# Kernel optimization log

Hardware: AMD Instinct MI355X
Metric: run time of the kernel (lower is better)

Reference implementation:

```python
import jax, jax.numpy as jnp
import numpy as np

NUM_HEADS = 4


def setup_inputs() -> dict:
    key = jax.random.key(0)
    ks = jax.random.split(key, 5)
    B, S, E = 32, 1024, 512
    T, Q = 128, 256
    src_encodings = jax.random.normal(ks[0], (B, S, E), dtype=jnp.float32)
    src_token_mask = jax.random.randint(ks[1], (B, S), 0, 2).astype(bool)
    query_vec = jax.random.normal(ks[2], (T, B, Q), dtype=jnp.float32)
    # torch Linear weights are (out_features, in_features)
    W_src = jax.random.normal(ks[3], (NUM_HEADS * Q, E), dtype=jnp.float32) * (1.0 / np.sqrt(E))
    W_opt = jax.random.normal(ks[4], (NUM_HEADS, Q), dtype=jnp.float32) * (1.0 / np.sqrt(Q))
    return {"src_encodings": src_encodings, "src_token_mask": src_token_mask,
            "query_vec": query_vec, "W_src": W_src, "W_opt": W_opt}


def reference(src_encodings, src_token_mask, query_vec, W_src, W_opt):
    B, S, _ = src_encodings.shape
    T = query_vec.shape[0]
    Q = query_vec.shape[2]
    # project + leaky_relu (torch default negative_slope=0.01), split into heads
    proj = jax.nn.leaky_relu(jnp.einsum('bse,fe->bsf', src_encodings, W_src))  # (B,S,H*Q)
    proj = proj.reshape(B, S, NUM_HEADS, Q)                                    # (B,S,H,Q)
    # per-head scores: (T,B,S,H)
    weights = jnp.einsum('bshq,tbq->tbsh', proj, query_vec)
    # head routing: argmax over options scores (T,B,H) -> top-1 head per (t,b)
    options_scores = jnp.einsum('tbq,hq->tbh', query_vec, W_opt)
    best = jnp.argmax(options_scores, axis=-1)                                 # (T,B)
    w = jnp.take_along_axis(weights, best[:, :, None, None], axis=-1)[..., 0]  # (T,B,S)
    # mask and softmax over source positions
    w = jnp.where(src_token_mask[None, :, :], -jnp.inf, w)
    return jax.nn.softmax(w, axis=-1)
```

## Files before the change

kernel.cpp:

```cpp
#include <hip/hip_runtime.h>
#include <hip/hip_bf16.h>
#include <math.h>

#define B_ 32
#define S_ 1024
#define E_ 512
#define T_ 128
#define Q_ 256
#define H_ 4
#define F_ (H_ * Q_)
#define M_ (B_ * S_)

typedef _Float16 f16x8 __attribute__((ext_vector_type(8)));
typedef float f32x4 __attribute__((ext_vector_type(4)));
typedef unsigned int uint32;

__device__ __forceinline__ float lrelu(float x) { return x > 0.0f ? x : 0.01f * x; }

__device__ __forceinline__ uint32 packh2(float a, float b) {
    union { _Float16 h[2]; uint32 u; } v;
    v.h[0] = (_Float16)a; v.h[1] = (_Float16)b;
    return v.u;
}
__device__ __forceinline__ unsigned short packh1(float a) {
    union { _Float16 h; unsigned short u; } v;
    v.h = (_Float16)a;
    return v.u;
}

#define GLOAD_LDS16(g, l)                                                       \
    __builtin_amdgcn_global_load_lds(                                           \
        (const __attribute__((address_space(1))) void*)(g),                     \
        (__attribute__((address_space(3))) void*)(l), 16, 0, 0)

#define SRC_BLOCKS 16384
#define W_BLOCKS   512
#define HS_BLOCKS  1024

__global__ __launch_bounds__(256) void prep_kernel(
    float* src, float* wsrc,
    const float* __restrict__ qv, const float* __restrict__ Wopt,
    int* __restrict__ best) {
    const int blk = blockIdx.x;
    if (blk < SRC_BLOCKS + W_BLOCKS) {
        float* base = (blk < SRC_BLOCKS) ? src : wsrc;
        const size_t woff = (size_t)((blk < SRC_BLOCKS) ? blk : (blk - SRC_BLOCKS)) * 16;
        const int tid = threadIdx.x;
        const size_t c = woff + (tid >> 4);
        const int j = tid & 15;
        float* wp = base + c * 64;
        float4 v = *(const float4*)(wp + j * 4);
        uint2 o = make_uint2(packh2(v.x, v.y), packh2(v.z, v.w));
        *(uint2*)((char*)wp + j * 8) = o;
    } else {
        const int wave = threadIdx.x >> 6, lane = threadIdx.x & 63;
        const int idx = (blk - SRC_BLOCKS - W_BLOCKS) * 4 + wave;
        const float4 qq = *(const float4*)(qv + (size_t)idx * Q_ + lane * 4);
        float s[4];
#pragma unroll
        for (int h = 0; h < 4; ++h) {
            float4 w = *(const float4*)(Wopt + h * Q_ + lane * 4);
            s[h] = qq.x * w.x + qq.y * w.y + qq.z * w.z + qq.w * w.w;
        }
#pragma unroll
        for (int off = 32; off >= 1; off >>= 1) {
#pragma unroll
            for (int h = 0; h < 4; ++h) s[h] += __shfl_down(s[h], off);
        }
        if (lane == 0) {
            int bh = 0; float bs = s[0];
            if (s[1] > bs) { bs = s[1]; bh = 1; }
            if (s[2] > bs) { bs = s[2]; bh = 2; }
            if (s[3] > bs) { bs = s[3]; bh = 3; }
            best[idx] = bh;
        }
    }
}

__global__ __launch_bounds__(256, 2) void proj_score_kernel(
    const unsigned char* __restrict__ Apk,
    const unsigned char* __restrict__ Wpk,
    const float* __restrict__ qv,
    const int* __restrict__ best,
    float* __restrict__ bufs)
{
    __shared__ uint4 smem4[4096];
    char* smem = (char*)smem4;

    const int bid = blockIdx.x;
    const int xcd = bid & 7;
    const int q_ = bid >> 3;
    const int bi = xcd * 32 + (q_ >> 3);
    const int bj = q_ & 7;

    const int tid = threadIdx.x;
    const int wave = tid >> 6, lane = tid & 63;
    const int wm = wave >> 1, wn = wave & 1;
    const int quad = lane >> 4;
    const int fr = lane & 15;
    const int xr = fr & 7;

    const size_t Abase = (size_t)(bi * 128) * 2048;
    const size_t Wbase = (size_t)(bj * 128) * 2048;

    const int r16 = lane >> 2;
    const int slot = lane & 3;
    const int sgb = ((slot ^ ((r16 >> 1) & 3)) & 3) * 16;
    const unsigned char* gA = Apk + Abase + (size_t)(wave * 32 + r16) * 2048 + sgb;
    const unsigned char* gW = Wpk + Wbase + (size_t)(wave * 32 + r16) * 2048 + sgb;

    const int koB = ((quad ^ ((fr >> 1) & 3)) & 3) * 16;
    const int aoff = (wm * 64 + fr) * 64 + koB;
    const int boff = (wn * 64 + fr) * 64 + koB;

    f32x4 acc[4][4] = {};

#define STAGE(bufb_, ks_) do {                                                 \
    const int hb_ = ((ks_) >> 1) * 256 + ((ks_) & 1) * 64;                     \
    _Pragma("unroll")                                                          \
    for (int c_ = 0; c_ < 2; ++c_) {                                           \
        const unsigned char* a_ = gA + (size_t)c_ * 16 * 2048 + hb_;           \
        const unsigned char* w_ = gW + (size_t)c_ * 16 * 2048 + hb_;           \
        char* l_ = smem + (bufb_) + wave * 2048 + c_ * 1024;                   \
        GLOAD_LDS16(a_, l_);                                                   \
        GLOAD_LDS16(w_, l_ + 8192);                                            \
    }                                                                          \
} while (0)

    STAGE(0, 0);
    STAGE(16384, 1);
    asm volatile("s_waitcnt vmcnt(4)" ::: "memory");
    __builtin_amdgcn_s_barrier();

    int cur = 0;
#pragma unroll 1
    for (int ks = 0; ks < 16; ++ks) {
        f16x8 ah[4], bh4[4];
#pragma unroll
        for (int i_ = 0; i_ < 4; ++i_) {
            ah[i_]  = *(const f16x8*)(smem + cur +        aoff + i_ * 1024);
            bh4[i_] = *(const f16x8*)(smem + cur + 8192 + boff + i_ * 1024);
        }
        asm volatile("s_waitcnt lgkmcnt(0)" ::: "memory");
        __builtin_amdgcn_s_barrier();
        if (ks < 14) STAGE(cur, ks + 2);
        __builtin_amdgcn_s_setprio(1);
#pragma unroll
        for (int i_ = 0; i_ < 4; ++i_)
#pragma unroll
            for (int j_ = 0; j_ < 4; ++j_) {
                acc[i_][j_] = __builtin_amdgcn_mfma_f32_16x16x32_f16(ah[i_], bh4[j_], acc[i_][j_], 0, 0, 0);
            }
        __builtin_amdgcn_s_setprio(0);
        if (ks < 14) {
            asm volatile("s_waitcnt vmcnt(4)" ::: "memory");
        } else if (ks == 14) {
            asm volatile("s_waitcnt vmcnt(0)" ::: "memory");
        }
        if (ks < 15) __builtin_amdgcn_s_barrier();
        cur ^= 16384;
    }

#undef STAGE

    const int b = bi >> 3;
    const int sbase = (bi & 7) * 128;
    const int h = bj >> 1;
    const int qoff = (bj & 1) * 128;
    float* buf = bufs + (size_t)(bj & 1) * ((size_t)T_ * B_ * S_);

    __syncthreads();
    int* tl = (int*)(smem + 49152);
    int* lcnt = (int*)(smem + 49152 + 512);
    if (tid == 0) *lcnt = 0;
    __syncthreads();
    if (tid < 128) {
        if (best[tid * B_ + b] == h) {
            int slot2 = atomicAdd(lcnt, 1);
            tl[slot2] = tid;
        }
    }
    __syncthreads();
    const int n = *lcnt;

    const int t_idx = tid >> 3, seg = tid & 7;

    for (int half = 0; half < 2; ++half) {
        if (wm == half) {
#pragma unroll
            for (int i = 0; i < 4; ++i) {
#pragma unroll
                for (int j = 0; j < 4; ++j) {
                    int col = wn * 64 + j * 16 + fr;
                    int g = col >> 3;
                    int cb = (col & 7) * 2;
#pragma unroll
                    for (int r = 0; r < 4; ++r) {
                        int rr = i * 16 + quad * 4 + r;
                        int gs = (g & 8) | ((g ^ rr) & 7);
                        *(unsigned short*)(smem + rr * 256 + gs * 16 + cb) =
                            packh1(lrelu(acc[i][j][r]));
                    }
                }
            }
        }
        __syncthreads();

        for (int tc = 0; tc < n; tc += 32) {
            int nn = min(32, n - tc);
            if (t_idx < nn) {
                int tt = tl[tc + t_idx];
                const float* qp = qv + ((size_t)tt * B_ + b) * Q_ + qoff + seg * 16;
                float4 f0 = *(const float4*)(qp);
                float4 f1 = *(const float4*)(qp + 4);
                float4 f2 = *(const float4*)(qp + 8);
                float4 f3 = *(const float4*)(qp + 12);
                uint4 h0 = make_uint4(packh2(f0.x, f0.y), packh2(f0.z, f0.w),
                                      packh2(f1.x, f1.y), packh2(f1.z, f1.w));
                uint4 h1 = make_uint4(packh2(f2.x, f2.y), packh2(f2.z, f2.w),
                                      packh2(f3.x, f3.y), packh2(f3.z, f3.w));
                int g0 = seg * 2, g1 = seg * 2 + 1;
                int gs0 = (g0 & 8) | ((g0 ^ t_idx) & 7);
                int gs1 = (g1 & 8) | ((g1 ^ t_idx) & 7);
                *(uint4*)(smem + 32768 + t_idx * 256 + gs0 * 16) = h0;
                *(uint4*)(smem + 32768 + t_idx * 256 + gs1 * 16) = h1;
            }
            __syncthreads();

            f32x4 sc0 = {0.f, 0.f, 0.f, 0.f}, sc1 = {0.f, 0.f, 0.f, 0.f};
#pragma unroll
            for (int ks = 0; ks < 4; ++ks) {
                int kb = ks * 4 + quad;
                int ko = ((kb & 8) | ((kb ^ xr) & 7)) * 16;
                int prow = wave * 16 + fr;
                f16x8 ph = *(const f16x8*)(smem + prow * 256 + ko);
                f16x8 qh0 = *(const f16x8*)(smem + 32768 + fr * 256 + ko);
                sc0 = __builtin_amdgcn_mfma_f32_16x16x32_f16(qh0, ph, sc0, 0, 0, 0);
                if (nn > 16) {
                    f16x8 qh1 = *(const f16x8*)(smem + 32768 + (16 + fr) * 256 + ko);
                    sc1 = __builtin_amdgcn_mfma_f32_16x16x32_f16(qh1, ph, sc1, 0, 0, 0);
                }
            }
            int sg = sbase + half * 64 + wave * 16 + fr;
#pragma unroll
            for (int r = 0; r < 4; ++r) {
                int t0 = quad * 4 + r;
                if (t0 < nn) {
                    int tg = tl[tc + t0];
                    buf[((size_t)tg * B_ + b) * S_ + sg] = sc0[r];
                }
                int t1 = 16 + quad * 4 + r;
                if (t1 < nn) {
                    int tg = tl[tc + t1];
                    buf[((size_t)tg * B_ + b) * S_ + sg] = sc1[r];
                }
            }
            __syncthreads();
        }
        __syncthreads();
    }
}

__global__ __launch_bounds__(256) void softmax_kernel(
    const float* __restrict__ bufs, float* __restrict__ out,
    const int* __restrict__ mask) {
    const int row = blockIdx.x;
    const int b = row & (B_ - 1);
    const float* w0 = bufs + (size_t)row * S_;
    const float* w1 = w0 + (size_t)T_ * B_ * S_;
    float* w = out + (size_t)row * S_;
    const int* mrow = mask + (size_t)b * S_;
    const int tid = threadIdx.x;

    float4 va = *(const float4*)(w0 + tid * 4);
    float4 vb = *(const float4*)(w1 + tid * 4);
    int4 mm = *(const int4*)(mrow + tid * 4);
    float x0 = mm.x ? -INFINITY : (va.x + vb.x);
    float x1 = mm.y ? -INFINITY : (va.y + vb.y);
    float x2 = mm.z ? -INFINITY : (va.z + vb.z);
    float x3 = mm.w ? -INFINITY : (va.w + vb.w);

    float lmax = fmaxf(fmaxf(x0, x1), fmaxf(x2, x3));
#pragma unroll
    for (int off = 32; off >= 1; off >>= 1)
        lmax = fmaxf(lmax, __shfl_down(lmax, off));

    __shared__ float redmax[4];
    __shared__ float redsum[4];
    const int wave = tid >> 6, lane = tid & 63;
    if (lane == 0) redmax[wave] = lmax;
    __syncthreads();
    float gmax = fmaxf(fmaxf(redmax[0], redmax[1]), fmaxf(redmax[2], redmax[3]));

    float e0 = mm.x ? 0.f : __expf(x0 - gmax);
    float e1 = mm.y ? 0.f : __expf(x1 - gmax);
    float e2 = mm.z ? 0.f : __expf(x2 - gmax);
    float e3 = mm.w ? 0.f : __expf(x3 - gmax);
    float lsum = e0 + e1 + e2 + e3;
#pragma unroll
    for (int off = 32; off >= 1; off >>= 1)
        lsum += __shfl_down(lsum, off);
    if (lane == 0) redsum[wave] = lsum;
    __syncthreads();
    float gsum = redsum[0] + redsum[1] + redsum[2] + redsum[3];
    float rinv = 1.0f / gsum;

    *(float4*)(w + tid * 4) = make_float4(e0 * rinv, e1 * rinv, e2 * rinv, e3 * rinv);
}

extern "C" void kernel_launch(void* const* d_in, const int* in_sizes, int n_in,
                              void* d_out, int out_size, void* d_ws, size_t ws_size,
                              hipStream_t stream) {
    float* src  = (float*)d_in[0];
    const int* mask = (const int*)d_in[1];
    const float* qv = (const float*)d_in[2];
    float* Wsrc = (float*)d_in[3];
    const float* Wopt = (const float*)d_in[4];
    float* out = (float*)d_out;

    float* bufs = (float*)d_ws;
    int* best = (int*)((char*)d_ws + 2 * (size_t)T_ * B_ * S_ * sizeof(float));

    hipLaunchKernelGGL(prep_kernel, dim3(SRC_BLOCKS + W_BLOCKS + HS_BLOCKS), dim3(256),
                       0, stream, src, Wsrc, qv, Wopt, best);
    hipLaunchKernelGGL(proj_score_kernel, dim3(2048), dim3(256), 0, stream,
                       (const unsigned char*)src, (const unsigned char*)Wsrc,
                       qv, best, bufs);
    hipLaunchKernelGGL(softmax_kernel, dim3(T_ * B_), dim3(256), 0, stream,
                       bufs, out, mask);
}
```

Baseline: 183.5 us.

## Widen GEMM tile to a full head so scores need no partial-sum buffer

The projection GEMM tile grows from 128x128 to 128x256 columns, so each block covers one whole head of Q=256. The score dot product then finishes inside one block, which drops the second partial-score buffer and the extra read-and-add in softmax. The fp32-to-fp16 prep pass also gives each thread four times as much data, using 16-byte stores. In exchange the GEMM uses more LDS and accumulator registers (acc[4][8]) and launches half as many blocks, which may lower occupancy.

```diff
diff --git a/kernel.cpp b/kernel.cpp
--- a/kernel.cpp
+++ b/kernel.cpp
@@ -33,28 +33,36 @@
         (const __attribute__((address_space(1))) void*)(g),                     \
         (__attribute__((address_space(3))) void*)(l), 16, 0, 0)
 
-#define SRC_BLOCKS 16384
-#define W_BLOCKS   512
-#define HS_BLOCKS  1024
+#define SRCW_BLOCKS 4096
+#define WW_BLOCKS   128
+#define HS_BLOCKS   1024
 
 __global__ __launch_bounds__(256) void prep_kernel(
     float* src, float* wsrc,
     const float* __restrict__ qv, const float* __restrict__ Wopt,
     int* __restrict__ best) {
     const int blk = blockIdx.x;
-    if (blk < SRC_BLOCKS + W_BLOCKS) {
-        float* base = (blk < SRC_BLOCKS) ? src : wsrc;
-        const size_t woff = (size_t)((blk < SRC_BLOCKS) ? blk : (blk - SRC_BLOCKS)) * 16;
+    if (blk < SRCW_BLOCKS + WW_BLOCKS) {
+        float* base = (blk < SRCW_BLOCKS) ? src : wsrc;
+        const size_t w0 = (size_t)((blk < SRCW_BLOCKS) ? blk : (blk - SRCW_BLOCKS)) * 64;
         const int tid = threadIdx.x;
-        const size_t c = woff + (tid >> 4);
-        const int j = tid & 15;
-        float* wp = base + c * 64;
-        float4 v = *(const float4*)(wp + j * 4);
-        uint2 o = make_uint2(packh2(v.x, v.y), packh2(v.z, v.w));
-        *(uint2*)((char*)wp + j * 8) = o;
+        const size_t c = w0 + (tid >> 2);
+        const int j = tid & 3;
+        const float* rp = base + c * 64 + j * 16;
+        float4 v0 = ((const float4*)rp)[0];
+        float4 v1 = ((const float4*)rp)[1];
+        float4 v2 = ((const float4*)rp)[2];
+        float4 v3 = ((const float4*)rp)[3];
+        uint4 o0 = make_uint4(packh2(v0.x, v0.y), packh2(v0.z, v0.w),
+                              packh2(v1.x, v1.y), packh2(v1.z, v1.w));
+        uint4 o1 = make_uint4(packh2(v2.x, v2.y), packh2(v2.z, v2.w),
+                              packh2(v3.x, v3.y), packh2(v3.z, v3.w));
+        char* op = (char*)(base + c * 64) + j * 32;
+        ((uint4*)op)[0] = o0;
+        ((uint4*)op)[1] = o1;
     } else {
         const int wave = threadIdx.x >> 6, lane = threadIdx.x & 63;
-        const int idx = (blk - SRC_BLOCKS - W_BLOCKS) * 4 + wave;
+        const int idx = (blk - SRCW_BLOCKS - WW_BLOCKS) * 4 + wave;
         const float4 qq = *(const float4*)(qv + (size_t)idx * Q_ + lane * 4);
         float s[4];
 #pragma unroll
@@ -84,14 +92,14 @@
     const int* __restrict__ best,
     float* __restrict__ bufs)
 {
-    __shared__ uint4 smem4[4096];
+    __shared__ uint4 smem4[4800];
     char* smem = (char*)smem4;
 
     const int bid = blockIdx.x;
     const int xcd = bid & 7;
     const int q_ = bid >> 3;
-    const int bi = xcd * 32 + (q_ >> 3);
-    const int bj = q_ & 7;
+    const int bi = xcd * 32 + (q_ >> 2);
+    const int bj = q_ & 3;
 
     const int tid = threadIdx.x;
     const int wave = tid >> 6, lane = tid & 63;
@@ -101,46 +109,49 @@
     const int xr = fr & 7;
 
     const size_t Abase = (size_t)(bi * 128) * 2048;
-    const size_t Wbase = (size_t)(bj * 128) * 2048;
+    const size_t Wbase = (size_t)(bj * 256) * 2048;
 
     const int r16 = lane >> 2;
     const int slot = lane & 3;
     const int sgb = ((slot ^ ((r16 >> 1) & 3)) & 3) * 16;
     const unsigned char* gA = Apk + Abase + (size_t)(wave * 32 + r16) * 2048 + sgb;
-    const unsigned char* gW = Wpk + Wbase + (size_t)(wave * 32 + r16) * 2048 + sgb;
+    const unsigned char* gW = Wpk + Wbase + (size_t)(wave * 64 + r16) * 2048 + sgb;
 
     const int koB = ((quad ^ ((fr >> 1) & 3)) & 3) * 16;
     const int aoff = (wm * 64 + fr) * 64 + koB;
-    const int boff = (wn * 64 + fr) * 64 + koB;
-
-    f32x4 acc[4][4] = {};
+    const int boff = (wn * 128 + fr) * 64 + koB;
+
+    f32x4 acc[4][8] = {};
 
 #define STAGE(bufb_, ks_) do {                                                 \
     const int hb_ = ((ks_) >> 1) * 256 + ((ks_) & 1) * 64;                     \
     _Pragma("unroll")                                                          \
     for (int c_ = 0; c_ < 2; ++c_) {                                           \
-        const unsigned char* a_ = gA + (size_t)c_ * 16 * 2048 + hb_;           \
-        const unsigned char* w_ = gW + (size_t)c_ * 16 * 2048 + hb_;           \
-        char* l_ = smem + (bufb_) + wave * 2048 + c_ * 1024;                   \
-        GLOAD_LDS16(a_, l_);                                                   \
-        GLOAD_LDS16(w_, l_ + 8192);                                            \
+        GLOAD_LDS16(gA + (size_t)c_ * 16 * 2048 + hb_,                         \
+                    smem + (bufb_) + (wave * 2 + c_) * 1024);                  \
+    }                                                                          \
+    _Pragma("unroll")                                                          \
+    for (int c_ = 0; c_ < 4; ++c_) {                                           \
+        GLOAD_LDS16(gW + (size_t)c_ * 16 * 2048 + hb_,                         \
+                    smem + (bufb_) + 8192 + (wave * 4 + c_) * 1024);           \
     }                                                                          \
 } while (0)
 
     STAGE(0, 0);
-    STAGE(16384, 1);
-    asm volatile("s_waitcnt vmcnt(4)" ::: "memory");
+    STAGE(24576, 1);
+    asm volatile("s_waitcnt vmcnt(6)" ::: "memory");
     __builtin_amdgcn_s_barrier();
 
     int cur = 0;
 #pragma unroll 1
     for (int ks = 0; ks < 16; ++ks) {
-        f16x8 ah[4], bh4[4];
-#pragma unroll
-        for (int i_ = 0; i_ < 4; ++i_) {
-            ah[i_]  = *(const f16x8*)(smem + cur +        aoff + i_ * 1024);
-            bh4[i_] = *(const f16x8*)(smem + cur + 8192 + boff + i_ * 1024);
-        }
+        f16x8 ah[4], bh8[8];
+#pragma unroll
+        for (int i_ = 0; i_ < 4; ++i_)
+            ah[i_] = *(const f16x8*)(smem + cur + aoff + i_ * 1024);
+#pragma unroll
+        for (int j_ = 0; j_ < 8; ++j_)
+            bh8[j_] = *(const f16x8*)(smem + cur + 8192 + boff + j_ * 1024);
         asm volatile("s_waitcnt lgkmcnt(0)" ::: "memory");
         __builtin_amdgcn_s_barrier();
         if (ks < 14) STAGE(cur, ks + 2);
@@ -148,34 +159,31 @@
 #pragma unroll
         for (int i_ = 0; i_ < 4; ++i_)
 #pragma unroll
-            for (int j_ = 0; j_ < 4; ++j_) {
-                acc[i_][j_] = __builtin_amdgcn_mfma_f32_16x16x32_f16(ah[i_], bh4[j_], acc[i_][j_], 0, 0, 0);
+            for (int j_ = 0; j_ < 8; ++j_) {
+                acc[i_][j_] = __builtin_amdgcn_mfma_f32_16x16x32_f16(ah[i_], bh8[j_], acc[i_][j_], 0, 0, 0);
             }
         __builtin_amdgcn_s_setprio(0);
         if (ks < 14) {
-            asm volatile("s_waitcnt vmcnt(4)" ::: "memory");
+            asm volatile("s_waitcnt vmcnt(6)" ::: "memory");
         } else if (ks == 14) {
             asm volatile("s_waitcnt vmcnt(0)" ::: "memory");
         }
         if (ks < 15) __builtin_amdgcn_s_barrier();
-        cur ^= 16384;
+        cur ^= 24576;
     }
 
 #undef STAGE
 
     const int b = bi >> 3;
     const int sbase = (bi & 7) * 128;
-    const int h = bj >> 1;
-    const int qoff = (bj & 1) * 128;
-    float* buf = bufs + (size_t)(bj & 1) * ((size_t)T_ * B_ * S_);
-
-    __syncthreads();
-    int* tl = (int*)(smem + 49152);
-    int* lcnt = (int*)(smem + 49152 + 512);
+
+    __syncthreads();
+    int* tl = (int*)(smem + 73728);
+    int* lcnt = (int*)(smem + 74240);
     if (tid == 0) *lcnt = 0;
     __syncthreads();
     if (tid < 128) {
-        if (best[tid * B_ + b] == h) {
+        if (best[tid * B_ + b] == bj) {
             int slot2 = atomicAdd(lcnt, 1);
             tl[slot2] = tid;
         }
@@ -183,79 +191,69 @@
     __syncthreads();
     const int n = *lcnt;
 
-    const int t_idx = tid >> 3, seg = tid & 7;
-
-    for (int half = 0; half < 2; ++half) {
-        if (wm == half) {
-#pragma unroll
-            for (int i = 0; i < 4; ++i) {
-#pragma unroll
-                for (int j = 0; j < 4; ++j) {
-                    int col = wn * 64 + j * 16 + fr;
-                    int g = col >> 3;
-                    int cb = (col & 7) * 2;
-#pragma unroll
-                    for (int r = 0; r < 4; ++r) {
-                        int rr = i * 16 + quad * 4 + r;
-                        int gs = (g & 8) | ((g ^ rr) & 7);
-                        *(unsigned short*)(smem + rr * 256 + gs * 16 + cb) =
-                            packh1(lrelu(acc[i][j][r]));
-                    }
+#pragma unroll
+    for (int i = 0; i < 4; ++i) {
+#pragma unroll
+        for (int j = 0; j < 8; ++j) {
+            int col = wn * 128 + j * 16 + fr;
+            int g = col >> 3;
+            int cb = (col & 7) * 2;
+#pragma unroll
+            for (int r = 0; r < 4; ++r) {
+                int rr = wm * 64 + i * 16 + quad * 4 + r;
+                int gs = (g & 24) | ((g ^ rr) & 7);
+                *(unsigned short*)(smem + rr * 512 + gs * 16 + cb) =
+                    packh1(lrelu(acc[i][j][r]));
+            }
+        }
+    }
+    __syncthreads();
+
+    const int t_idx = tid >> 4, seg = tid & 15;
+
+    for (int tc = 0; tc < n; tc += 16) {
+        int nn = min(16, n - tc);
+        if (t_idx < nn) {
+            int tt = tl[tc + t_idx];
+            const float* qp = qv + ((size_t)tt * B_ + b) * Q_ + seg * 16;
+            float4 f0 = *(const float4*)(qp);
+            float4 f1 = *(const float4*)(qp + 4);
+            float4 f2 = *(const float4*)(qp + 8);
+            float4 f3 = *(const float4*)(qp + 12);
+            uint4 h0 = make_uint4(packh2(f0.x, f0.y), packh2(f0.z, f0.w),
+                                  packh2(f1.x, f1.y), packh2(f1.z, f1.w));
+            uint4 h1 = make_uint4(packh2(f2.x, f2.y), packh2(f2.z, f2.w),
+                                  packh2(f3.x, f3.y), packh2(f3.z, f3.w));
+            int g0 = seg * 2, g1 = seg * 2 + 1;
+            int gs0 = (g0 & 24) | ((g0 ^ t_idx) & 7);
+            int gs1 = (g1 & 24) | ((g1 ^ t_idx) & 7);
+            *(uint4*)(smem + 65536 + t_idx * 512 + gs0 * 16) = h0;
+            *(uint4*)(smem + 65536 + t_idx * 512 + gs1 * 16) = h1;
+        }
+        __syncthreads();
+
+#pragma unroll
+        for (int sub = 0; sub < 2; ++sub) {
+            const int sblk = wave * 2 + sub;
+            const int srow = sblk * 16 + fr;
+            f32x4 sc = {0.f, 0.f, 0.f, 0.f};
+#pragma unroll
+            for (int ks2 = 0; ks2 < 8; ++ks2) {
+                int kb = ks2 * 4 + quad;
+                int ko = ((kb & 24) | ((kb ^ xr) & 7)) * 16;
+                f16x8 ph = *(const f16x8*)(smem + srow * 512 + ko);
+                f16x8 qh = *(const f16x8*)(smem + 65536 + fr * 512 + ko);
+                sc = __builtin_amdgcn_mfma_f32_16x16x32_f16(qh, ph, sc, 0, 0, 0);
+            }
+            int sg = sbase + sblk * 16 + fr;
+#pragma unroll
+            for (int r = 0; r < 4; ++r) {
+                int tloc = quad * 4 + r;
+                if (tloc < nn) {
+                    int tg = tl[tc + tloc];
+                    bufs[((size_t)tg * B_ + b) * S_ + sg] = sc[r];
                 }
             }
-        }
-        __syncthreads();
-
-        for (int tc = 0; tc < n; tc += 32) {
-            int nn = min(32, n - tc);
-            if (t_idx < nn) {
-                int tt = tl[tc + t_idx];
-                const float* qp = qv + ((size_t)tt * B_ + b) * Q_ + qoff + seg * 16;
-                float4 f0 = *(const float4*)(qp);
-                float4 f1 = *(const float4*)(qp + 4);
-                float4 f2 = *(const float4*)(qp + 8);
-                float4 f3 = *(const float4*)(qp + 12);
-                uint4 h0 = make_uint4(packh2(f0.x, f0.y), packh2(f0.z, f0.w),
-                                      packh2(f1.x, f1.y), packh2(f1.z, f1.w));
-                uint4 h1 = make_uint4(packh2(f2.x, f2.y), packh2(f2.z, f2.w),
-                                      packh2(f3.x, f3.y), packh2(f3.z, f3.w));
-                int g0 = seg * 2, g1 = seg * 2 + 1;
-                int gs0 = (g0 & 8) | ((g0 ^ t_idx) & 7);
-                int gs1 = (g1 & 8) | ((g1 ^ t_idx) & 7);
-                *(uint4*)(smem + 32768 + t_idx * 256 + gs0 * 16) = h0;
-                *(uint4*)(smem + 32768 + t_idx * 256 + gs1 * 16) = h1;
-            }
-            __syncthreads();
-
-            f32x4 sc0 = {0.f, 0.f, 0.f, 0.f}, sc1 = {0.f, 0.f, 0.f, 0.f};
-#pragma unroll
-            for (int ks = 0; ks < 4; ++ks) {
-                int kb = ks * 4 + quad;
-                int ko = ((kb & 8) | ((kb ^ xr) & 7)) * 16;
-                int prow = wave * 16 + fr;
-                f16x8 ph = *(const f16x8*)(smem + prow * 256 + ko);
-                f16x8 qh0 = *(const f16x8*)(smem + 32768 + fr * 256 + ko);
-                sc0 = __builtin_amdgcn_mfma_f32_16x16x32_f16(qh0, ph, sc0, 0, 0, 0);
-                if (nn > 16) {
-                    f16x8 qh1 = *(const f16x8*)(smem + 32768 + (16 + fr) * 256 + ko);
-                    sc1 = __builtin_amdgcn_mfma_f32_16x16x32_f16(qh1, ph, sc1, 0, 0, 0);
-                }
-            }
-            int sg = sbase + half * 64 + wave * 16 + fr;
-#pragma unroll
-            for (int r = 0; r < 4; ++r) {
-                int t0 = quad * 4 + r;
-                if (t0 < nn) {
-                    int tg = tl[tc + t0];
-                    buf[((size_t)tg * B_ + b) * S_ + sg] = sc0[r];
-                }
-                int t1 = 16 + quad * 4 + r;
-                if (t1 < nn) {
-                    int tg = tl[tc + t1];
-                    buf[((size_t)tg * B_ + b) * S_ + sg] = sc1[r];
-                }
-            }
-            __syncthreads();
         }
         __syncthreads();
     }
@@ -267,18 +265,16 @@
     const int row = blockIdx.x;
     const int b = row & (B_ - 1);
     const float* w0 = bufs + (size_t)row * S_;
-    const float* w1 = w0 + (size_t)T_ * B_ * S_;
     float* w = out + (size_t)row * S_;
     const int* mrow = mask + (size_t)b * S_;
     const int tid = threadIdx.x;
 
     float4 va = *(const float4*)(w0 + tid * 4);
-    float4 vb = *(const float4*)(w1 + tid * 4);
     int4 mm = *(const int4*)(mrow + tid * 4);
-    float x0 = mm.x ? -INFINITY : (va.x + vb.x);
-    float x1 = mm.y ? -INFINITY : (va.y + vb.y);
-    float x2 = mm.z ? -INFINITY : (va.z + vb.z);
-    float x3 = mm.w ? -INFINITY : (va.w + vb.w);
+    float x0 = mm.x ? -INFINITY : va.x;
+    float x1 = mm.y ? -INFINITY : va.y;
+    float x2 = mm.z ? -INFINITY : va.z;
+    float x3 = mm.w ? -INFINITY : va.w;
 
     float lmax = fmaxf(fmaxf(x0, x1), fmaxf(x2, x3));
 #pragma unroll
@@ -319,11 +315,11 @@
     float* out = (float*)d_out;
 
     float* bufs = (float*)d_ws;
-    int* best = (int*)((char*)d_ws + 2 * (size_t)T_ * B_ * S_ * sizeof(float));
-
-    hipLaunchKernelGGL(prep_kernel, dim3(SRC_BLOCKS + W_BLOCKS + HS_BLOCKS), dim3(256),
+    int* best = (int*)((char*)d_ws + (size_t)T_ * B_ * S_ * sizeof(float));
+
+    hipLaunchKernelGGL(prep_kernel, dim3(SRCW_BLOCKS + WW_BLOCKS + HS_BLOCKS), dim3(256),
                        0, stream, src, Wsrc, qv, Wopt, best);
-    hipLaunchKernelGGL(proj_score_kernel, dim3(2048), dim3(256), 0, stream,
+    hipLaunchKernelGGL(proj_score_kernel, dim3(1024), dim3(256), 0, stream,
                        (const unsigned char*)src, (const unsigned char*)Wsrc,
                        qv, best, bufs);
     hipLaunchKernelGGL(softmax_kernel, dim3(T_ * B_), dim3(256), 0, stream,
```

After: 165.8 us. -9.6%, faster.
